# Optimization experiments

Measured on AMD Instinct MI355X. Metric: run time of the kernel, lower is better.

Reference implementation:

```python
import jax, jax.numpy as jnp
import numpy as np

S, B, D, H = 256, 32, 512, 512

def setup_inputs() -> dict:
    key = jax.random.key(0)
    ks = jax.random.split(key, 14)
    return {
        "x": jax.random.normal(ks[0], (S, B, D), jnp.float32),
        "hidden_prev": jax.random.normal(ks[1], (1, B, H), jnp.float32) * 0.1,
        "Z_state": jax.random.normal(ks[2], (1, B, H, D), jnp.float32) * 0.01,
        "F_state": jax.random.normal(ks[3], (1, B, H, D), jnp.float32) * 0.01,
        "wz_state": jax.random.normal(ks[4], (1, B, H), jnp.float32) * 0.01,
        "wf_state": jax.random.normal(ks[5], (1, B, H), jnp.float32) * 0.01,
        "bz_state": jax.random.normal(ks[6], (1, B, H), jnp.float32) * 0.01,
        "bf_state": jax.random.normal(ks[7], (1, B, H), jnp.float32) * 0.01,
        "wm_z": jax.random.normal(ks[8], (H, D), jnp.float32) * 0.1,
        "wm_f": jax.random.normal(ks[9], (H, D), jnp.float32) * 0.1,
        "wv_z": jax.random.normal(ks[10], (1, H), jnp.float32) * 0.1,
        "wv_f": jax.random.normal(ks[11], (1, H), jnp.float32) * 0.1,
        "bias_z": jax.random.normal(ks[12], (1, H), jnp.float32) * 0.1,
        "bias_f": jax.random.normal(ks[13], (1, H), jnp.float32) * 0.1,
    }

def reference(x, hidden_prev, Z_state, F_state, wz_state, wf_state, bz_state, bf_state,
              wm_z, wm_f, wv_z, wv_f, bias_z, bias_f):
    # Input projections for both gates, done once: [S,B,H]
    pre_z = jnp.einsum('sbd,hd->sbh', x, wm_z)
    pre_f = jnp.einsum('sbd,hd->sbh', x, wm_f)

    def step(carry, inp):
        cell, Z, Fm, wz, wf, bz, bf = carry
        x_t, pz, pf = inp  # [B,D], [B,H], [B,H]
        z = jnp.tanh(pz + wv_z * cell + bias_z)          # [B,H]
        f = jax.nn.sigmoid(pf + wv_f * cell + bias_f)    # [B,H]
        zf = (1.0 - f) * (1.0 - z * z)
        fz = (cell - z) * (1.0 - f) * f
        common = f + zf * wv_z + fz * wv_f
        # RTRL sensitivity updates (outer products over [B,H,D])
        Zn = common[..., None] * Z + zf[..., None] * x_t[:, None, :]
        Fn = common[..., None] * Fm + fz[..., None] * x_t[:, None, :]
        wzn = cell * zf + common * wz
        wfn = cell * fz + common * wf
        bzn = zf + common * bz
        bfn = fz + common * bf
        new_cell = cell * f + (1.0 - f) * z
        return (new_cell, Zn, Fn, wzn, wfn, bzn, bfn), new_cell

    carry0 = (hidden_prev[0], Z_state[0], F_state[0],
              wz_state[0], wf_state[0], bz_state[0], bf_state[0])
    carry, cells = jax.lax.scan(step, carry0, (x, pre_z, pre_f))
    new_cell, Zn, Fn, wzn, wfn, bzn, bfn = carry
    return (cells, new_cell[None], Zn[None], Fn[None],
            wzn[None], wfn[None], bzn[None], bfn[None])
```

## Files before the change

kernel.cpp:

```cpp
#include <hip/hip_runtime.h>
#include <math.h>

namespace {

typedef short short8 __attribute__((ext_vector_type(8)));
typedef float floatx4 __attribute__((ext_vector_type(4)));
typedef unsigned int uint32;
typedef unsigned short ushort16;
typedef unsigned long long u64;

constexpr int S = 256, B = 32, D = 512, H = 512;
constexpr int BH = B * H;
constexpr int M1 = S * B;
constexpr int XN = M1 * D;
constexpr int WN = H * D;
constexpr int SBH = S * BH;

__device__ __forceinline__ uint32 f2bf(float f) {
  uint32 x = __float_as_uint(f);
  return (x + 0x7fffu + ((x >> 16) & 1u)) >> 16;
}

__device__ __forceinline__ float fast_sigmoid(float x) {
  float e = __expf(-x);
  return __builtin_amdgcn_rcpf(1.0f + e);
}
__device__ __forceinline__ float fast_tanh(float x) {
  float e = __expf(-2.0f * x);
  return fmaf(2.0f, __builtin_amdgcn_rcpf(1.0f + e), -1.0f);
}

__global__ __launch_bounds__(256) void convert_kernel(
    const float* __restrict__ x, const float* __restrict__ wmz,
    const float* __restrict__ wmf, ushort16* __restrict__ xb,
    ushort16* __restrict__ wmzb, ushort16* __restrict__ wmfb) {
  int i = (blockIdx.x * 256 + threadIdx.x) * 8;
  const float* src;
  ushort16* dst;
  int off;
  if (i < XN) {
    src = x; dst = xb; off = i;
  } else if (i < XN + WN) {
    src = wmz; dst = wmzb; off = i - XN;
  } else {
    src = wmf; dst = wmfb; off = i - XN - WN;
  }
  float4 a = *(const float4*)&src[off];
  float4 b = *(const float4*)&src[off + 4];
  uint4 o;
  o.x = f2bf(a.x) | (f2bf(a.y) << 16);
  o.y = f2bf(a.z) | (f2bf(a.w) << 16);
  o.z = f2bf(b.x) | (f2bf(b.y) << 16);
  o.w = f2bf(b.z) | (f2bf(b.w) << 16);
  *(uint4*)&dst[off] = o;
}

constexpr int LDA = 72;
__global__ __launch_bounds__(256) void proj_gemm(
    const ushort16* __restrict__ xb, const ushort16* __restrict__ wmzb,
    const ushort16* __restrict__ wmfb, float2* __restrict__ pzf) {
  __shared__ ushort16 As[128 * LDA];
  __shared__ ushort16 Bzs[64 * LDA];
  __shared__ ushort16 Bfs[64 * LDA];
  const int tid = threadIdx.x;
  const int m0 = blockIdx.x * 128;
  const int n0 = blockIdx.y * 64;
  const int w = tid >> 6, l = tid & 63;
  const int lr = l & 15, lg = l >> 4;
  floatx4 accz[2][4], accf[2][4];
#pragma unroll
  for (int m = 0; m < 2; ++m)
#pragma unroll
    for (int n = 0; n < 4; ++n) {
      accz[m][n] = 0;
      accf[m][n] = 0;
    }
  const int sr = tid >> 3;
  const int sc = (tid & 7) * 8;
  for (int k0 = 0; k0 < D; k0 += 64) {
    __syncthreads();
#pragma unroll
    for (int p = 0; p < 4; ++p) {
      int r = sr + 32 * p;
      *(short8*)&As[r * LDA + sc] =
          *(const short8*)&xb[(size_t)(m0 + r) * D + k0 + sc];
    }
#pragma unroll
    for (int p = 0; p < 2; ++p) {
      int r = sr + 32 * p;
      *(short8*)&Bzs[r * LDA + sc] =
          *(const short8*)&wmzb[(size_t)(n0 + r) * D + k0 + sc];
      *(short8*)&Bfs[r * LDA + sc] =
          *(const short8*)&wmfb[(size_t)(n0 + r) * D + k0 + sc];
    }
    __syncthreads();
#pragma unroll
    for (int kk = 0; kk < 2; ++kk) {
      const int kb = kk * 32 + lg * 8;
      short8 a0 = *(const short8*)&As[(32 * w + lr) * LDA + kb];
      short8 a1 = *(const short8*)&As[(32 * w + 16 + lr) * LDA + kb];
#pragma unroll
      for (int n = 0; n < 4; ++n) {
        short8 bz = *(const short8*)&Bzs[(16 * n + lr) * LDA + kb];
        short8 bf = *(const short8*)&Bfs[(16 * n + lr) * LDA + kb];
        accz[0][n] = __builtin_amdgcn_mfma_f32_16x16x32_bf16(a0, bz, accz[0][n], 0, 0, 0);
        accz[1][n] = __builtin_amdgcn_mfma_f32_16x16x32_bf16(a1, bz, accz[1][n], 0, 0, 0);
        accf[0][n] = __builtin_amdgcn_mfma_f32_16x16x32_bf16(a0, bf, accf[0][n], 0, 0, 0);
        accf[1][n] = __builtin_amdgcn_mfma_f32_16x16x32_bf16(a1, bf, accf[1][n], 0, 0, 0);
      }
    }
  }
#pragma unroll
  for (int m = 0; m < 2; ++m)
#pragma unroll
    for (int n = 0; n < 4; ++n)
#pragma unroll
      for (int j = 0; j < 4; ++j) {
        int row = m0 + 32 * w + 16 * m + lg * 4 + j;
        int col = n0 + 16 * n + lr;
        pzf[(size_t)row * H + col] = make_float2(accz[m][n][j], accf[m][n][j]);
      }
}

#define STEP_BODY(J)                                                       \
    const float z = fast_tanh(fmaf(wvz, cell, pzv));                       \
    const float f = fast_sigmoid(fmaf(wvf, cell, pfv));                    \
    const float zf = (1.0f - f) * (1.0f - z * z);                          \
    const float fz = (cell - z) * (1.0f - f) * f;                          \
    const float common = f + zf * wvz + fz * wvf;                          \
    wz = fmaf(common, wz, cell * zf);                                      \
    wf = fmaf(common, wf, cell * fz);                                      \
    bz = fmaf(common, bz, zf);                                             \
    bf = fmaf(common, bf, fz);                                             \
    cell = fmaf(f, cell - z, z);                                           \
    const size_t ti = (size_t)(t0 + (J)) * BH;                             \
    cp[ti] = cell;                                                         \
    pz[ti] = make_float2(                                                  \
        __uint_as_float(f2bf(zf) | (f2bf(fz) << 16)), common);

#define STEP_L(J, Q)                                                       \
  {                                                                        \
    const float pzv = Q.x + bsz, pfv = Q.y + bsf;                          \
    Q = pz[(size_t)(t0 + 16 + (J)) * BH];                                  \
    STEP_BODY(J)                                                           \
  }

#define STEP_N(J, Q)                                                       \
  {                                                                        \
    const float pzv = Q.x + bsz, pfv = Q.y + bsf;                          \
    STEP_BODY(J)                                                           \
  }

__global__ __launch_bounds__(64, 1) void scan_fwd(
    const float* __restrict__ hidden_prev, const float* __restrict__ wz0,
    const float* __restrict__ wf0, const float* __restrict__ bz0,
    const float* __restrict__ bf0, const float* __restrict__ wvz_,
    const float* __restrict__ wvf_, const float* __restrict__ bsz_,
    const float* __restrict__ bsf_, float2* pzf_,
    float* __restrict__ out_cells, float* __restrict__ out_newcell,
    float* __restrict__ out_wzn, float* __restrict__ out_wfn,
    float* __restrict__ out_bzn, float* __restrict__ out_bfn) {
  const int bh = blockIdx.x * 64 + threadIdx.x;
  const int h = bh & (H - 1);
  float cell = hidden_prev[bh];
  float wz = wz0[bh], wf = wf0[bh], bz = bz0[bh], bf = bf0[bh];
  const float wvz = wvz_[h], wvf = wvf_[h], bsz = bsz_[h], bsf = bsf_[h];
  float2* pz = pzf_ + bh;
  float* cp = out_cells + bh;

  float2 q0 = pz[(size_t)0 * BH], q1 = pz[(size_t)1 * BH];
  float2 q2 = pz[(size_t)2 * BH], q3 = pz[(size_t)3 * BH];
  float2 q4 = pz[(size_t)4 * BH], q5 = pz[(size_t)5 * BH];
  float2 q6 = pz[(size_t)6 * BH], q7 = pz[(size_t)7 * BH];
  float2 q8 = pz[(size_t)8 * BH], q9 = pz[(size_t)9 * BH];
  float2 q10 = pz[(size_t)10 * BH], q11 = pz[(size_t)11 * BH];
  float2 q12 = pz[(size_t)12 * BH], q13 = pz[(size_t)13 * BH];
  float2 q14 = pz[(size_t)14 * BH], q15 = pz[(size_t)15 * BH];

  for (int t0 = 0; t0 < S - 16; t0 += 16) {
    STEP_L(0, q0)  STEP_L(1, q1)  STEP_L(2, q2)  STEP_L(3, q3)
    STEP_L(4, q4)  STEP_L(5, q5)  STEP_L(6, q6)  STEP_L(7, q7)
    STEP_L(8, q8)  STEP_L(9, q9)  STEP_L(10, q10) STEP_L(11, q11)
    STEP_L(12, q12) STEP_L(13, q13) STEP_L(14, q14) STEP_L(15, q15)
  }
  {
    const int t0 = S - 16;
    STEP_N(0, q0)  STEP_N(1, q1)  STEP_N(2, q2)  STEP_N(3, q3)
    STEP_N(4, q4)  STEP_N(5, q5)  STEP_N(6, q6)  STEP_N(7, q7)
    STEP_N(8, q8)  STEP_N(9, q9)  STEP_N(10, q10) STEP_N(11, q11)
    STEP_N(12, q12) STEP_N(13, q13) STEP_N(14, q14) STEP_N(15, q15)
  }
  out_newcell[bh] = cell;
  out_wzn[bh] = wz;
  out_wfn[bh] = wf;
  out_bzn[bh] = bz;
  out_bfn[bh] = bf;
}

__global__ __launch_bounds__(1024) void suffix_kernel(
    const float2* __restrict__ pzfc, uint32* __restrict__ azf,
    float* __restrict__ P0_out) {
  __shared__ float prods[16][65];
  const int bh_l = threadIdx.x & 63;
  const int c = threadIdx.x >> 6;
  const int bh = blockIdx.x * 64 + bh_l;
  const float2* p = pzfc + bh;
  float2 v[16];
#pragma unroll
  for (int i = 0; i < 16; ++i) v[i] = p[(size_t)(c * 16 + i) * BH];
  float L = 1.0f;
#pragma unroll
  for (int i = 0; i < 16; ++i) L *= v[i].y;
  prods[c][bh_l] = L;
  __syncthreads();
  float run = 1.0f;
#pragma unroll
  for (int cc = 1; cc < 16; ++cc)
    if (cc > c) run *= prods[cc][bh_l];
  uint32* az = azf + bh;
#pragma unroll
  for (int i = 15; i >= 0; --i) {
    const int t = c * 16 + i;
    const uint32 w32 = __float_as_uint(v[i].x);
    const float zf = __uint_as_float((w32 & 0xffffu) << 16);
    const float fz = __uint_as_float(w32 & 0xffff0000u);
    az[(size_t)t * BH] = f2bf(zf * run) | (f2bf(fz * run) << 16);
    run *= v[i].y;
  }
  if (c == 0) P0_out[bh] = run;
}

constexpr int LDT = 132;
constexpr int LDX = 68;
__global__ __launch_bounds__(256) void out_gemm(
    const uint32* __restrict__ azf, const ushort16* __restrict__ xb,
    const float* __restrict__ P0, const float* __restrict__ Z0,
    const float* __restrict__ F0, float* __restrict__ Zn,
    float* __restrict__ Fn) {
  __shared__ ushort16 Azs[64 * LDT];
  __shared__ ushort16 Afs[64 * LDT];
  __shared__ ushort16 Xs[64 * LDX];
  const int tid = threadIdx.x;
  const int h0 = blockIdx.x * 128;
  const int d0 = blockIdx.y * 64;
  const int b = blockIdx.z;
  const int w = tid >> 6, l = tid & 63;
  const int lr = l & 15, lg = l >> 4;
  floatx4 accz[2][4], accf[2][4];
#pragma unroll
  for (int m = 0; m < 2; ++m)
#pragma unroll
    for (int n = 0; n < 4; ++n) {
      accz[m][n] = 0;
      accf[m][n] = 0;
    }
  const int at = tid >> 5;
  const int ah = (tid & 31) * 4;
  const int xt = tid >> 3;
  const int xc = (tid & 7) * 8;

  for (int t0 = 0; t0 < S; t0 += 64) {
    __syncthreads();
#pragma unroll
    for (int p = 0; p < 8; ++p) {
      const int t = at + 8 * p;
      const uint4 v =
          *(const uint4*)&azf[(size_t)(t0 + t) * BH + b * H + h0 + ah];
      const int base = t * LDT + ah;
      Azs[base + 0] = (ushort16)(v.x & 0xffffu);
      Afs[base + 0] = (ushort16)(v.x >> 16);
      Azs[base + 1] = (ushort16)(v.y & 0xffffu);
      Afs[base + 1] = (ushort16)(v.y >> 16);
      Azs[base + 2] = (ushort16)(v.z & 0xffffu);
      Afs[base + 2] = (ushort16)(v.z >> 16);
      Azs[base + 3] = (ushort16)(v.w & 0xffffu);
      Afs[base + 3] = (ushort16)(v.w >> 16);
    }
#pragma unroll
    for (int p = 0; p < 2; ++p) {
      const int t = xt + 32 * p;
      const size_t g = (size_t)(t0 + t) * BH + (size_t)b * D + xc + d0;
      u64 v0 = *(const u64*)&xb[g];
      u64 v1 = *(const u64*)&xb[g + 4];
      *(u64*)&Xs[t * LDX + xc] = v0;
      *(u64*)&Xs[t * LDX + xc + 4] = v1;
    }
    __syncthreads();
#pragma unroll
    for (int kk = 0; kk < 2; ++kk) {
      const int kb = kk * 32 + lg * 8;
      short8 az0, az1, af0, af1, xf[4];
#pragma unroll
      for (int e = 0; e < 8; ++e) {
        const int ro = (kb + e) * LDT;
        az0[e] = (short)Azs[ro + 32 * w + lr];
        az1[e] = (short)Azs[ro + 32 * w + 16 + lr];
        af0[e] = (short)Afs[ro + 32 * w + lr];
        af1[e] = (short)Afs[ro + 32 * w + 16 + lr];
        const int rx = (kb + e) * LDX;
        xf[0][e] = (short)Xs[rx + lr];
        xf[1][e] = (short)Xs[rx + 16 + lr];
        xf[2][e] = (short)Xs[rx + 32 + lr];
        xf[3][e] = (short)Xs[rx + 48 + lr];
      }
#pragma unroll
      for (int n = 0; n < 4; ++n) {
        accz[0][n] = __builtin_amdgcn_mfma_f32_16x16x32_bf16(az0, xf[n], accz[0][n], 0, 0, 0);
        accz[1][n] = __builtin_amdgcn_mfma_f32_16x16x32_bf16(az1, xf[n], accz[1][n], 0, 0, 0);
        accf[0][n] = __builtin_amdgcn_mfma_f32_16x16x32_bf16(af0, xf[n], accf[0][n], 0, 0, 0);
        accf[1][n] = __builtin_amdgcn_mfma_f32_16x16x32_bf16(af1, xf[n], accf[1][n], 0, 0, 0);
      }
    }
  }
#pragma unroll
  for (int m = 0; m < 2; ++m)
#pragma unroll
    for (int j = 0; j < 4; ++j) {
      const int row = h0 + 32 * w + 16 * m + lg * 4 + j;
      const float p0 = P0[b * H + row];
#pragma unroll
      for (int n = 0; n < 4; ++n) {
        const int col = d0 + 16 * n + lr;
        const size_t idx = ((size_t)b * H + row) * D + col;
        Zn[idx] = fmaf(p0, Z0[idx], accz[m][n][j]);
        Fn[idx] = fmaf(p0, F0[idx], accf[m][n][j]);
      }
    }
}

}

extern "C" void kernel_launch(void* const* d_in, const int* in_sizes, int n_in,
                              void* d_out, int out_size, void* d_ws,
                              size_t ws_size, hipStream_t stream) {
  const float* x = (const float*)d_in[0];
  const float* hidden_prev = (const float*)d_in[1];
  const float* Z_state = (const float*)d_in[2];
  const float* F_state = (const float*)d_in[3];
  const float* wz_state = (const float*)d_in[4];
  const float* wf_state = (const float*)d_in[5];
  const float* bz_state = (const float*)d_in[6];
  const float* bf_state = (const float*)d_in[7];
  const float* wm_z = (const float*)d_in[8];
  const float* wm_f = (const float*)d_in[9];
  const float* wv_z = (const float*)d_in[10];
  const float* wv_f = (const float*)d_in[11];
  const float* bias_z = (const float*)d_in[12];
  const float* bias_f = (const float*)d_in[13];

  float2* pzf = (float2*)d_ws;
  uint32* azf = (uint32*)(pzf + SBH);
  ushort16* xb = (ushort16*)(azf + SBH);
  ushort16* wmzb = xb + XN;
  ushort16* wmfb = wmzb + WN;
  float* P0 = (float*)(wmfb + WN);

  float* out = (float*)d_out;
  float* out_cells = out;
  float* out_newcell = out + SBH;
  float* out_Zn = out_newcell + BH;
  float* out_Fn = out_Zn + (size_t)BH * D;
  float* out_wzn = out_Fn + (size_t)BH * D;
  float* out_wfn = out_wzn + BH;
  float* out_bzn = out_wfn + BH;
  float* out_bfn = out_bzn + BH;

  convert_kernel<<<(XN + 2 * WN) / 8 / 256, 256, 0, stream>>>(
      x, wm_z, wm_f, xb, wmzb, wmfb);
  proj_gemm<<<dim3(M1 / 128, H / 64), 256, 0, stream>>>(xb, wmzb, wmfb, pzf);
  scan_fwd<<<BH / 64, 64, 0, stream>>>(
      hidden_prev, wz_state, wf_state, bz_state, bf_state, wv_z, wv_f, bias_z,
      bias_f, pzf, out_cells, out_newcell, out_wzn, out_wfn, out_bzn,
      out_bfn);
  suffix_kernel<<<BH / 64, 1024, 0, stream>>>(pzf, azf, P0);
  out_gemm<<<dim3(H / 128, D / 64, B), 256, 0, stream>>>(
      azf, xb, P0, Z_state, F_state, out_Zn, out_Fn);
}
```

Measured before the change: 114.5 us.

## Store out_gemm operands K-contiguous via transposes to enable vector LDS fragment loads

Adds a transpose kernel that writes x as bf16 in [B,D,S] layout, and makes the suffix kernel transpose its coefficient output through LDS into separate [B,H,S] Az and Af arrays. With the time dimension contiguous, out_gemm can load MFMA fragments with 16-byte short8 LDS reads instead of eight scalar 16-bit gathers per fragment. proj_gemm now converts x to bf16 inline rather than reading a pre-converted copy. The cost is an extra transpose pass over x and a large LDS buffer in the suffix kernel, which may reduce its occupancy.

```diff
diff --git a/kernel.cpp b/kernel.cpp
--- a/kernel.cpp
+++ b/kernel.cpp
@@ -6,13 +6,12 @@
 typedef short short8 __attribute__((ext_vector_type(8)));
 typedef float floatx4 __attribute__((ext_vector_type(4)));
 typedef unsigned int uint32;
-typedef unsigned short ushort16;
+typedef unsigned short u16;
 typedef unsigned long long u64;
 
 constexpr int S = 256, B = 32, D = 512, H = 512;
 constexpr int BH = B * H;
 constexpr int M1 = S * B;
-constexpr int XN = M1 * D;
 constexpr int WN = H * D;
 constexpr int SBH = S * BH;
 
@@ -30,20 +29,17 @@
   return fmaf(2.0f, __builtin_amdgcn_rcpf(1.0f + e), -1.0f);
 }
 
-__global__ __launch_bounds__(256) void convert_kernel(
-    const float* __restrict__ x, const float* __restrict__ wmz,
-    const float* __restrict__ wmf, ushort16* __restrict__ xb,
-    ushort16* __restrict__ wmzb, ushort16* __restrict__ wmfb) {
+__global__ __launch_bounds__(256) void convert_w(
+    const float* __restrict__ wmz, const float* __restrict__ wmf,
+    u16* __restrict__ wmzb, u16* __restrict__ wmfb) {
   int i = (blockIdx.x * 256 + threadIdx.x) * 8;
   const float* src;
-  ushort16* dst;
+  u16* dst;
   int off;
-  if (i < XN) {
-    src = x; dst = xb; off = i;
-  } else if (i < XN + WN) {
-    src = wmz; dst = wmzb; off = i - XN;
+  if (i < WN) {
+    src = wmz; dst = wmzb; off = i;
   } else {
-    src = wmf; dst = wmfb; off = i - XN - WN;
+    src = wmf; dst = wmfb; off = i - WN;
   }
   float4 a = *(const float4*)&src[off];
   float4 b = *(const float4*)&src[off + 4];
@@ -55,13 +51,45 @@
   *(uint4*)&dst[off] = o;
 }
 
+__global__ __launch_bounds__(256) void xpose_kernel(
+    const float* __restrict__ x, u16* __restrict__ XT) {
+  __shared__ float lds[64][65];
+  const int s0 = blockIdx.x * 64;
+  const int d0 = blockIdx.y * 64;
+  const int b = blockIdx.z;
+  const int r = threadIdx.x >> 4;
+  const int c4 = (threadIdx.x & 15) * 4;
+#pragma unroll
+  for (int p = 0; p < 4; ++p) {
+    const int rr = r + p * 16;
+    float4 v = *(const float4*)&x[(size_t)(s0 + rr) * (B * D) +
+                                  (size_t)b * D + d0 + c4];
+    lds[c4 + 0][rr] = v.x;
+    lds[c4 + 1][rr] = v.y;
+    lds[c4 + 2][rr] = v.z;
+    lds[c4 + 3][rr] = v.w;
+  }
+  __syncthreads();
+#pragma unroll
+  for (int p = 0; p < 4; ++p) {
+    const int dr = r + p * 16;
+    const float v0 = lds[dr][c4 + 0];
+    const float v1 = lds[dr][c4 + 1];
+    const float v2 = lds[dr][c4 + 2];
+    const float v3 = lds[dr][c4 + 3];
+    u64 o = (u64)f2bf(v0) | ((u64)f2bf(v1) << 16) | ((u64)f2bf(v2) << 32) |
+            ((u64)f2bf(v3) << 48);
+    *(u64*)&XT[((size_t)b * D + d0 + dr) * S + s0 + c4] = o;
+  }
+}
+
 constexpr int LDA = 72;
 __global__ __launch_bounds__(256) void proj_gemm(
-    const ushort16* __restrict__ xb, const ushort16* __restrict__ wmzb,
-    const ushort16* __restrict__ wmfb, float2* __restrict__ pzf) {
-  __shared__ ushort16 As[128 * LDA];
-  __shared__ ushort16 Bzs[64 * LDA];
-  __shared__ ushort16 Bfs[64 * LDA];
+    const float* __restrict__ x, const u16* __restrict__ wmzb,
+    const u16* __restrict__ wmfb, float2* __restrict__ pzf) {
+  __shared__ u16 As[128 * LDA];
+  __shared__ u16 Bzs[64 * LDA];
+  __shared__ u16 Bfs[64 * LDA];
   const int tid = threadIdx.x;
   const int m0 = blockIdx.x * 128;
   const int n0 = blockIdx.y * 64;
@@ -81,13 +109,20 @@
     __syncthreads();
 #pragma unroll
     for (int p = 0; p < 4; ++p) {
-      int r = sr + 32 * p;
-      *(short8*)&As[r * LDA + sc] =
-          *(const short8*)&xb[(size_t)(m0 + r) * D + k0 + sc];
+      const int r = sr + 32 * p;
+      const float* xp = &x[(size_t)(m0 + r) * D + k0 + sc];
+      float4 a = *(const float4*)xp;
+      float4 b = *(const float4*)(xp + 4);
+      uint4 o;
+      o.x = f2bf(a.x) | (f2bf(a.y) << 16);
+      o.y = f2bf(a.z) | (f2bf(a.w) << 16);
+      o.z = f2bf(b.x) | (f2bf(b.y) << 16);
+      o.w = f2bf(b.z) | (f2bf(b.w) << 16);
+      *(uint4*)&As[r * LDA + sc] = o;
     }
 #pragma unroll
     for (int p = 0; p < 2; ++p) {
-      int r = sr + 32 * p;
+      const int r = sr + 32 * p;
       *(short8*)&Bzs[r * LDA + sc] =
           *(const short8*)&wmzb[(size_t)(n0 + r) * D + k0 + sc];
       *(short8*)&Bfs[r * LDA + sc] =
@@ -198,9 +233,10 @@
 }
 
 __global__ __launch_bounds__(1024) void suffix_kernel(
-    const float2* __restrict__ pzfc, uint32* __restrict__ azf,
-    float* __restrict__ P0_out) {
+    const float2* __restrict__ pzfc, u16* __restrict__ AzT,
+    u16* __restrict__ AfT, float* __restrict__ P0_out) {
   __shared__ float prods[16][65];
+  __shared__ uint32 tl[S * 65];
   const int bh_l = threadIdx.x & 63;
   const int c = threadIdx.x >> 6;
   const int bh = blockIdx.x * 64 + bh_l;
@@ -217,33 +253,51 @@
 #pragma unroll
   for (int cc = 1; cc < 16; ++cc)
     if (cc > c) run *= prods[cc][bh_l];
-  uint32* az = azf + bh;
 #pragma unroll
   for (int i = 15; i >= 0; --i) {
     const int t = c * 16 + i;
     const uint32 w32 = __float_as_uint(v[i].x);
     const float zf = __uint_as_float((w32 & 0xffffu) << 16);
     const float fz = __uint_as_float(w32 & 0xffff0000u);
-    az[(size_t)t * BH] = f2bf(zf * run) | (f2bf(fz * run) << 16);
+    tl[t * 65 + bh_l] = f2bf(zf * run) | (f2bf(fz * run) << 16);
     run *= v[i].y;
   }
   if (c == 0) P0_out[bh] = run;
-}
-
-constexpr int LDT = 132;
-constexpr int LDX = 68;
+  __syncthreads();
+  const size_t base = (size_t)blockIdx.x * 64 * S;
+#pragma unroll
+  for (int it = 0; it < 4; ++it) {
+    const int qi = it * 1024 + threadIdx.x;
+    const int r = qi >> 6;
+    const int qt = (qi & 63) * 4;
+    const uint32 a0 = tl[(qt + 0) * 65 + r];
+    const uint32 a1 = tl[(qt + 1) * 65 + r];
+    const uint32 a2 = tl[(qt + 2) * 65 + r];
+    const uint32 a3 = tl[(qt + 3) * 65 + r];
+    u64 lo = (u64)(a0 & 0xffffu) | ((u64)(a1 & 0xffffu) << 16) |
+             ((u64)(a2 & 0xffffu) << 32) | ((u64)(a3 & 0xffffu) << 48);
+    u64 hi = (u64)(a0 >> 16) | ((u64)(a1 >> 16) << 16) |
+             ((u64)(a2 >> 16) << 32) | ((u64)(a3 >> 16) << 48);
+    *(u64*)&AzT[base + (size_t)r * S + qt] = lo;
+    *(u64*)&AfT[base + (size_t)r * S + qt] = hi;
+  }
+}
+
 __global__ __launch_bounds__(256) void out_gemm(
-    const uint32* __restrict__ azf, const ushort16* __restrict__ xb,
-    const float* __restrict__ P0, const float* __restrict__ Z0,
-    const float* __restrict__ F0, float* __restrict__ Zn,
-    float* __restrict__ Fn) {
-  __shared__ ushort16 Azs[64 * LDT];
-  __shared__ ushort16 Afs[64 * LDT];
-  __shared__ ushort16 Xs[64 * LDX];
+    const u16* __restrict__ AzT, const u16* __restrict__ AfT,
+    const u16* __restrict__ XT, const float* __restrict__ P0,
+    const float* __restrict__ Z0, const float* __restrict__ F0,
+    float* __restrict__ Zn, float* __restrict__ Fn) {
+  __shared__ u16 Azs[128 * LDA];
+  __shared__ u16 Afs[128 * LDA];
+  __shared__ u16 Xs[64 * LDA];
   const int tid = threadIdx.x;
   const int h0 = blockIdx.x * 128;
   const int d0 = blockIdx.y * 64;
   const int b = blockIdx.z;
+  const u16* Az = AzT + (size_t)b * H * S;
+  const u16* Af = AfT + (size_t)b * H * S;
+  const u16* Xb = XT + (size_t)b * D * S;
   const int w = tid >> 6, l = tid & 63;
   const int lr = l & 15, lg = l >> 4;
   floatx4 accz[2][4], accf[2][4];
@@ -254,61 +308,39 @@
       accz[m][n] = 0;
       accf[m][n] = 0;
     }
-  const int at = tid >> 5;
-  const int ah = (tid & 31) * 4;
-  const int xt = tid >> 3;
-  const int xc = (tid & 7) * 8;
-
+  const int sr = tid >> 3;
+  const int sc = (tid & 7) * 8;
   for (int t0 = 0; t0 < S; t0 += 64) {
     __syncthreads();
 #pragma unroll
-    for (int p = 0; p < 8; ++p) {
-      const int t = at + 8 * p;
-      const uint4 v =
-          *(const uint4*)&azf[(size_t)(t0 + t) * BH + b * H + h0 + ah];
-      const int base = t * LDT + ah;
-      Azs[base + 0] = (ushort16)(v.x & 0xffffu);
-      Afs[base + 0] = (ushort16)(v.x >> 16);
-      Azs[base + 1] = (ushort16)(v.y & 0xffffu);
-      Afs[base + 1] = (ushort16)(v.y >> 16);
-      Azs[base + 2] = (ushort16)(v.z & 0xffffu);
-      Afs[base + 2] = (ushort16)(v.z >> 16);
-      Azs[base + 3] = (ushort16)(v.w & 0xffffu);
-      Afs[base + 3] = (ushort16)(v.w >> 16);
+    for (int p = 0; p < 4; ++p) {
+      const int r = sr + 32 * p;
+      *(short8*)&Azs[r * LDA + sc] =
+          *(const short8*)&Az[(size_t)(h0 + r) * S + t0 + sc];
+      *(short8*)&Afs[r * LDA + sc] =
+          *(const short8*)&Af[(size_t)(h0 + r) * S + t0 + sc];
     }
 #pragma unroll
     for (int p = 0; p < 2; ++p) {
-      const int t = xt + 32 * p;
-      const size_t g = (size_t)(t0 + t) * BH + (size_t)b * D + xc + d0;
-      u64 v0 = *(const u64*)&xb[g];
-      u64 v1 = *(const u64*)&xb[g + 4];
-      *(u64*)&Xs[t * LDX + xc] = v0;
-      *(u64*)&Xs[t * LDX + xc + 4] = v1;
+      const int r = sr + 32 * p;
+      *(short8*)&Xs[r * LDA + sc] =
+          *(const short8*)&Xb[(size_t)(d0 + r) * S + t0 + sc];
     }
     __syncthreads();
 #pragma unroll
     for (int kk = 0; kk < 2; ++kk) {
       const int kb = kk * 32 + lg * 8;
-      short8 az0, az1, af0, af1, xf[4];
-#pragma unroll
-      for (int e = 0; e < 8; ++e) {
-        const int ro = (kb + e) * LDT;
-        az0[e] = (short)Azs[ro + 32 * w + lr];
-        az1[e] = (short)Azs[ro + 32 * w + 16 + lr];
-        af0[e] = (short)Afs[ro + 32 * w + lr];
-        af1[e] = (short)Afs[ro + 32 * w + 16 + lr];
-        const int rx = (kb + e) * LDX;
-        xf[0][e] = (short)Xs[rx + lr];
-        xf[1][e] = (short)Xs[rx + 16 + lr];
-        xf[2][e] = (short)Xs[rx + 32 + lr];
-        xf[3][e] = (short)Xs[rx + 48 + lr];
-      }
+      short8 az0 = *(const short8*)&Azs[(32 * w + lr) * LDA + kb];
+      short8 az1 = *(const short8*)&Azs[(32 * w + 16 + lr) * LDA + kb];
+      short8 af0 = *(const short8*)&Afs[(32 * w + lr) * LDA + kb];
+      short8 af1 = *(const short8*)&Afs[(32 * w + 16 + lr) * LDA + kb];
 #pragma unroll
       for (int n = 0; n < 4; ++n) {
-        accz[0][n] = __builtin_amdgcn_mfma_f32_16x16x32_bf16(az0, xf[n], accz[0][n], 0, 0, 0);
-        accz[1][n] = __builtin_amdgcn_mfma_f32_16x16x32_bf16(az1, xf[n], accz[1][n], 0, 0, 0);
-        accf[0][n] = __builtin_amdgcn_mfma_f32_16x16x32_bf16(af0, xf[n], accf[0][n], 0, 0, 0);
-        accf[1][n] = __builtin_amdgcn_mfma_f32_16x16x32_bf16(af1, xf[n], accf[1][n], 0, 0, 0);
+        short8 xf = *(const short8*)&Xs[(16 * n + lr) * LDA + kb];
+        accz[0][n] = __builtin_amdgcn_mfma_f32_16x16x32_bf16(az0, xf, accz[0][n], 0, 0, 0);
+        accz[1][n] = __builtin_amdgcn_mfma_f32_16x16x32_bf16(az1, xf, accz[1][n], 0, 0, 0);
+        accf[0][n] = __builtin_amdgcn_mfma_f32_16x16x32_bf16(af0, xf, accf[0][n], 0, 0, 0);
+        accf[1][n] = __builtin_amdgcn_mfma_f32_16x16x32_bf16(af1, xf, accf[1][n], 0, 0, 0);
       }
     }
   }
@@ -349,10 +381,11 @@
   const float* bias_f = (const float*)d_in[13];
 
   float2* pzf = (float2*)d_ws;
-  uint32* azf = (uint32*)(pzf + SBH);
-  ushort16* xb = (ushort16*)(azf + SBH);
-  ushort16* wmzb = xb + XN;
-  ushort16* wmfb = wmzb + WN;
+  u16* AzT = (u16*)(pzf + SBH);
+  u16* AfT = AzT + SBH;
+  u16* XT = AfT + SBH;
+  u16* wmzb = XT + SBH;
+  u16* wmfb = wmzb + WN;
   float* P0 = (float*)(wmfb + WN);
 
   float* out = (float*)d_out;
@@ -365,14 +398,14 @@
   float* out_bzn = out_wfn + BH;
   float* out_bfn = out_bzn + BH;
 
-  convert_kernel<<<(XN + 2 * WN) / 8 / 256, 256, 0, stream>>>(
-      x, wm_z, wm_f, xb, wmzb, wmfb);
-  proj_gemm<<<dim3(M1 / 128, H / 64), 256, 0, stream>>>(xb, wmzb, wmfb, pzf);
+  convert_w<<<2 * WN / 8 / 256, 256, 0, stream>>>(wm_z, wm_f, wmzb, wmfb);
+  xpose_kernel<<<dim3(S / 64, D / 64, B), 256, 0, stream>>>(x, XT);
+  proj_gemm<<<dim3(M1 / 128, H / 64), 256, 0, stream>>>(x, wmzb, wmfb, pzf);
   scan_fwd<<<BH / 64, 64, 0, stream>>>(
       hidden_prev, wz_state, wf_state, bz_state, bf_state, wv_z, wv_f, bias_z,
       bias_f, pzf, out_cells, out_newcell, out_wzn, out_wfn, out_bzn,
       out_bfn);
-  suffix_kernel<<<BH / 64, 1024, 0, stream>>>(pzf, azf, P0);
+  suffix_kernel<<<BH / 64, 1024, 0, stream>>>(pzf, AzT, AfT, P0);
   out_gemm<<<dim3(H / 128, D / 64, B), 256, 0, stream>>>(
-      azf, xb, P0, Z_state, F_state, out_Zn, out_Fn);
-}
+      AzT, AfT, XT, P0, Z_state, F_state, out_Zn, out_Fn);
+}
```

Result: slower. 143.9 us (+25.7%).
